# Optimization experiments

Measured on AMD Instinct MI355X. Metric: run time of the kernel, lower is better.

## Reference

```python
import jax, jax.numpy as jnp
import numpy as np

B, F, U, O, A, H = 8192, 1024, 512, 3, 6, 4  # batch, features, nb_units, nb_opponents, actions, heads
HD = U // H  # head dim


def setup_inputs() -> dict:
    key = jax.random.key(0)
    ks = jax.random.split(key, 12)
    s = 0.02
    rn = lambda k, shape: jax.random.normal(k, shape, jnp.float32) * s
    return {
        "features": jax.random.normal(ks[0], (B, F), jnp.float32),
        # agent latent Linear
        "W_al": rn(ks[1], (U, F)), "b_al": jnp.zeros((U,), jnp.float32),
        # MultiheadAttention in_proj (q,k,v stacked) and out_proj
        "W_in": rn(ks[2], (3 * U, U)), "b_in": jnp.zeros((3 * U,), jnp.float32),
        "W_out": rn(ks[3], (U, U)), "b_out": jnp.zeros((U,), jnp.float32),
        # agent head / policy / value
        "W_ah": rn(ks[4], (U, 2 * U)), "b_ah": jnp.zeros((U,), jnp.float32),
        "W_ap": rn(ks[5], (A, U)), "b_ap": jnp.zeros((A,), jnp.float32),
        "W_av": rn(ks[6], (1, U)), "b_av": jnp.zeros((1,), jnp.float32),
        # per-opponent stacks: latent, head, policy, value
        "W_ol": rn(ks[7], (O, U, F)), "b_ol": jnp.zeros((O, U), jnp.float32),
        "W_oh": rn(ks[8], (O, U, U)), "b_oh": jnp.zeros((O, U), jnp.float32),
        "W_op": rn(ks[9], (O, A, U)), "b_op": jnp.zeros((O, A), jnp.float32),
        "W_ov": rn(ks[10], (O, 1, U)), "b_ov": jnp.zeros((O, 1), jnp.float32),
    }


def reference(features, W_al, b_al, W_in, b_in, W_out, b_out, W_ah, b_ah,
              W_ap, b_ap, W_av, b_av, W_ol, b_ol, W_oh, b_oh, W_op, b_op, W_ov, b_ov):
    elu = jax.nn.elu
    # agent + per-opponent latents (per-opponent linears as one grouped GEMM)
    agent_latent = elu(features @ W_al.T + b_al)                                # [B,U]
    opp_lat = elu(jnp.einsum('bf,ouf->obu', features, W_ol) + b_ol[:, None, :])  # [O,B,U]

    # torch.nn.MultiheadAttention: query=[1,B,U] (agent), key=value=[O,B,U] (opponents)
    Wq, Wk, Wv = W_in[:U], W_in[U:2 * U], W_in[2 * U:]
    bq, bk, bv = b_in[:U], b_in[U:2 * U], b_in[2 * U:]
    q = (agent_latent @ Wq.T + bq).reshape(B, H, HD) * (1.0 / np.sqrt(HD))      # [B,H,HD]
    k = (jnp.einsum('obu,vu->obv', opp_lat, Wk) + bk).reshape(O, B, H, HD)
    v = (jnp.einsum('obu,vu->obv', opp_lat, Wv) + bv).reshape(O, B, H, HD)
    scores = jnp.einsum('bhd,obhd->bho', q, k)                                  # [B,H,O]
    w = jax.nn.softmax(scores, axis=-1)
    attn = jnp.einsum('bho,obhd->bhd', w, v).reshape(B, U)
    attn_out = attn @ W_out.T + b_out                                           # [B,U]
    opponents_influences = w.mean(axis=1)                                       # [B,O] (avg over heads)

    # agent head / policy / value
    cat = jnp.concatenate([agent_latent, attn_out], axis=1)                     # [B,2U]
    agent_head = elu(cat @ W_ah.T + b_ah)
    agent_policy = agent_head @ W_ap.T + b_ap                                   # [B,A]
    agent_value = agent_head @ W_av.T + b_av                                    # [B,1]

    # per-opponent head / policy / value (grouped GEMMs)
    opp_heads = elu(jnp.einsum('obu,ovu->obv', opp_lat, W_oh) + b_oh[:, None, :])  # [O,B,U]
    opponents_policies = jnp.einsum('obu,oau->boa', opp_heads, W_op) + b_op[None]   # [B,O,A]
    opponents_values = jnp.einsum('obu,ocu->boc', opp_heads, W_ov) + b_ov[None]     # [B,O,1]

    return (agent_policy, agent_value, opponents_policies, opponents_values, opponents_influences)
```

## Files before the change

### kernel.cpp

```cpp
#include <hip/hip_runtime.h>

typedef unsigned short u16;
typedef __bf16 bf16x8 __attribute__((ext_vector_type(8)));
typedef float f32x4 __attribute__((ext_vector_type(4)));

#define Bsz 8192
#define Fdim 1024
#define Udim 512
#define Odim 3
#define Adim 6
#define Hdim 4

#define OFF_FEAT   0
#define OFF_WAL    8388608
#define OFF_WIN    8912896
#define OFF_WOUT   9699328
#define OFF_WAH    9961472
#define OFF_WOL    10485760
#define OFF_WOH    12058624
#define OFF_CAT    12845056
#define OFF_OPP    21233664
#define OFF_Q      33816576
#define OFF_KV     38010880
#define OFF_ATT    63176704
#define OFF_AGH    67371008
#define OFF_OPH    71565312

#define OUT_AP 0
#define OUT_AV 49152
#define OUT_OP 57344
#define OUT_OV 204800
#define OUT_IN 229376

__device__ __forceinline__ u16 f2bf(float f) {
  return __builtin_bit_cast(u16, (__bf16)f);
}
__device__ __forceinline__ float bf2f(u16 u) {
  return (float)__builtin_bit_cast(__bf16, u);
}

__device__ __forceinline__ void gload16(const u16* g, u16* s) {
  __builtin_amdgcn_global_load_lds(
      (const __attribute__((address_space(1))) unsigned int*)g,
      (__attribute__((address_space(3))) unsigned int*)s, 16, 0, 0);
}

#define CV_E0 2097152
#define CV_E1 2228224
#define CV_E2 2424832
#define CV_E3 2490368
#define CV_E4 2621440
#define CV_E5 3014656
#define CV_E6 3211264
__global__ __launch_bounds__(256) void convert_all(
    const float* __restrict__ f, const float* __restrict__ wal,
    const float* __restrict__ win, const float* __restrict__ wout,
    const float* __restrict__ wah, const float* __restrict__ wol,
    const float* __restrict__ woh, u16* __restrict__ dst) {
  int i = blockIdx.x * 256 + threadIdx.x;
  if (i >= CV_E6) return;
  const float* src;
  int base;
  if (i < CV_E0)      { src = f;    base = 0; }
  else if (i < CV_E1) { src = wal;  base = CV_E0; }
  else if (i < CV_E2) { src = win;  base = CV_E1; }
  else if (i < CV_E3) { src = wout; base = CV_E2; }
  else if (i < CV_E4) { src = wah;  base = CV_E3; }
  else if (i < CV_E5) { src = wol;  base = CV_E4; }
  else                { src = woh;  base = CV_E5; }
  float4 v = ((const float4*)src)[i - base];
  ushort4 o;
  o.x = f2bf(v.x); o.y = f2bf(v.y); o.z = f2bf(v.z); o.w = f2bf(v.w);
  ((ushort4*)dst)[i] = o;
}

template <int BN, bool ELU>
__global__ __launch_bounds__(256) void gemm_bt(
    const u16* __restrict__ A, const u16* __restrict__ Bw, u16* __restrict__ C,
    const float* __restrict__ bias, int K, int lda, int ldb, int ldc,
    long sAz, long sBz, long sCz, int sbz, float scale) {
  constexpr int BM = 128, BK = 32;
  constexpr int NI = BN / 32;
  __shared__ __align__(16) u16 As[BM * BK];
  __shared__ __align__(16) u16 Bs[BN * BK];
  const int wave = threadIdx.x >> 6, lane = threadIdx.x & 63;
  const int z = blockIdx.z;
  A += (size_t)z * sAz;
  Bw += (size_t)z * sBz;
  C += (size_t)z * sCz;
  bias += (size_t)z * sbz;
  const int tM = blockIdx.y * BM, tN = blockIdx.x * BN;
  const int wr = wave >> 1, wc = wave & 1;

  f32x4 acc[4][NI];
#pragma unroll
  for (int i = 0; i < 4; i++)
#pragma unroll
    for (int j = 0; j < NI; j++) acc[i][j] = (f32x4){0.f, 0.f, 0.f, 0.f};

  const int srow = lane >> 2;
  const int scol = (lane & 3) * 8;

  for (int k0 = 0; k0 < K; k0 += BK) {
    __syncthreads();
#pragma unroll
    for (int i = 0; i < 2; ++i) {
      int r = wave * 32 + i * 16;
      gload16(A + (size_t)(tM + r + srow) * lda + k0 + scol, &As[r * BK]);
    }
#pragma unroll
    for (int i = 0; i < BN / 64; ++i) {
      int r = (wave * (BN / 64) + i) * 16;
      gload16(Bw + (size_t)(tN + r + srow) * ldb + k0 + scol, &Bs[r * BK]);
    }
    __syncthreads();
    bf16x8 af[4], bfr[NI];
#pragma unroll
    for (int mi = 0; mi < 4; mi++)
      af[mi] = *(const bf16x8*)&As[(wr * 64 + mi * 16 + (lane & 15)) * BK + (lane >> 4) * 8];
#pragma unroll
    for (int ni = 0; ni < NI; ni++)
      bfr[ni] = *(const bf16x8*)&Bs[(wc * (BN / 2) + ni * 16 + (lane & 15)) * BK + (lane >> 4) * 8];
#pragma unroll
    for (int mi = 0; mi < 4; mi++)
#pragma unroll
      for (int ni = 0; ni < NI; ni++)
        acc[mi][ni] = __builtin_amdgcn_mfma_f32_16x16x32_bf16(af[mi], bfr[ni], acc[mi][ni], 0, 0, 0);
  }

#pragma unroll
  for (int ni = 0; ni < NI; ni++) {
    int col = tN + wc * (BN / 2) + ni * 16 + (lane & 15);
    float bv = bias[col];
#pragma unroll
    for (int mi = 0; mi < 4; mi++) {
      int row0 = tM + wr * 64 + mi * 16 + (lane >> 4) * 4;
#pragma unroll
      for (int r = 0; r < 4; r++) {
        float v = (acc[mi][ni][r] + bv) * scale;
        if (ELU) v = v > 0.f ? v : (__expf(v) - 1.f);
        C[(size_t)(row0 + r) * ldc + col] = f2bf(v);
      }
    }
  }
}

__global__ __launch_bounds__(256) void attn_kernel(
    const u16* __restrict__ q, const u16* __restrict__ kv,
    u16* __restrict__ attn, float* __restrict__ influ) {
  const int wave = threadIdx.x >> 6, lane = threadIdx.x & 63;
  const int b = blockIdx.x * 4 + wave;
  const size_t qb = (size_t)b * 512;
  float wacc0 = 0.f, wacc1 = 0.f, wacc2 = 0.f;
#pragma unroll
  for (int h = 0; h < 4; ++h) {
    const int off = h * 128 + lane * 2;
    ushort2 qu = *(const ushort2*)(q + qb + off);
    float qx = bf2f(qu.x), qy = bf2f(qu.y);
    float s[3];
#pragma unroll
    for (int o = 0; o < 3; ++o) {
      ushort2 ku = *(const ushort2*)(kv + (size_t)o * (Bsz * 1024) + (size_t)b * 1024 + off);
      float p = qx * bf2f(ku.x) + qy * bf2f(ku.y);
#pragma unroll
      for (int d = 32; d; d >>= 1) p += __shfl_xor(p, d, 64);
      s[o] = p;
    }
    float m = fmaxf(s[0], fmaxf(s[1], s[2]));
    float e0 = __expf(s[0] - m), e1 = __expf(s[1] - m), e2 = __expf(s[2] - m);
    float inv = 1.f / (e0 + e1 + e2);
    float w0 = e0 * inv, w1 = e1 * inv, w2 = e2 * inv;
    wacc0 += w0; wacc1 += w1; wacc2 += w2;
    float ax = 0.f, ay = 0.f;
#pragma unroll
    for (int o = 0; o < 3; ++o) {
      float w = (o == 0) ? w0 : (o == 1) ? w1 : w2;
      ushort2 vu = *(const ushort2*)(kv + (size_t)o * (Bsz * 1024) + (size_t)b * 1024 + 512 + off);
      ax += w * bf2f(vu.x);
      ay += w * bf2f(vu.y);
    }
    ushort2 st; st.x = f2bf(ax); st.y = f2bf(ay);
    *(ushort2*)(attn + qb + off) = st;
  }
  if (lane == 0) {
    influ[b * 3 + 0] = wacc0 * 0.25f;
    influ[b * 3 + 1] = wacc1 * 0.25f;
    influ[b * 3 + 2] = wacc2 * 0.25f;
  }
}

__global__ __launch_bounds__(256) void heads_kernel(
    const u16* __restrict__ ah, const u16* __restrict__ oh,
    const float* __restrict__ Wap, const float* __restrict__ bap,
    const float* __restrict__ Wav, const float* __restrict__ bav,
    const float* __restrict__ Wop, const float* __restrict__ bop,
    const float* __restrict__ Wov, const float* __restrict__ bov,
    float* __restrict__ out) {
  __shared__ float sW[14336];
  for (int i = threadIdx.x; i < 14336; i += 256) {
    int s = i / 3584, rem = i - s * 3584;
    float v;
    if (s == 0) {
      v = (rem < 3072) ? Wap[rem] : Wav[rem - 3072];
    } else {
      int o = s - 1;
      v = (rem < 3072) ? Wop[o * 3072 + rem] : Wov[o * 512 + (rem - 3072)];
    }
    sW[i] = v;
  }
  __syncthreads();
  const int wave = threadIdx.x >> 6, lane = threadIdx.x & 63;
  const int kq = lane & 7, r = lane >> 3;
  const int b = blockIdx.x * 32 + wave * 8 + r;

  const u16* srcs[4] = {ah + (size_t)b * 512,
                        oh + (size_t)b * 512,
                        oh + (size_t)(Bsz + b) * 512,
                        oh + (size_t)(2 * Bsz + b) * 512};
  bf16x8 a[4][8];
#pragma unroll
  for (int s = 0; s < 4; s++)
#pragma unroll
    for (int c = 0; c < 8; c++)
      a[s][c] = *(const bf16x8*)(srcs[s] + c * 64 + kq * 8);

#pragma unroll
  for (int s = 0; s < 4; s++) {
#pragma unroll
    for (int p = 0; p < 7; p++) {
      const float* w = &sW[s * 3584 + p * 512 + kq * 8];
      float acc = 0.f;
#pragma unroll
      for (int c = 0; c < 8; c++) {
#pragma unroll
        for (int j = 0; j < 8; j++)
          acc += (float)a[s][c][j] * w[c * 64 + j];
      }
      acc += __shfl_xor(acc, 1, 64);
      acc += __shfl_xor(acc, 2, 64);
      acc += __shfl_xor(acc, 4, 64);
      if (kq == p) {
        if (s == 0) {
          if (p < 6) out[OUT_AP + b * 6 + p] = acc + bap[p];
          else       out[OUT_AV + b] = acc + bav[0];
        } else {
          int o = s - 1;
          if (p < 6) out[OUT_OP + b * 18 + o * 6 + p] = acc + bop[o * 6 + p];
          else       out[OUT_OV + b * 3 + o] = acc + bov[o];
        }
      }
    }
  }
}

extern "C" void kernel_launch(void* const* d_in, const int* in_sizes, int n_in,
                              void* d_out, int out_size, void* d_ws, size_t ws_size,
                              hipStream_t stream) {
  (void)in_sizes; (void)n_in; (void)out_size; (void)ws_size;
  const float* f     = (const float*)d_in[0];
  const float* W_al  = (const float*)d_in[1];
  const float* b_al  = (const float*)d_in[2];
  const float* W_in  = (const float*)d_in[3];
  const float* b_in  = (const float*)d_in[4];
  const float* W_out = (const float*)d_in[5];
  const float* b_out = (const float*)d_in[6];
  const float* W_ah  = (const float*)d_in[7];
  const float* b_ah  = (const float*)d_in[8];
  const float* W_ap  = (const float*)d_in[9];
  const float* b_ap  = (const float*)d_in[10];
  const float* W_av  = (const float*)d_in[11];
  const float* b_av  = (const float*)d_in[12];
  const float* W_ol  = (const float*)d_in[13];
  const float* b_ol  = (const float*)d_in[14];
  const float* W_oh  = (const float*)d_in[15];
  const float* b_oh  = (const float*)d_in[16];
  const float* W_op  = (const float*)d_in[17];
  const float* b_op  = (const float*)d_in[18];
  const float* W_ov  = (const float*)d_in[19];
  const float* b_ov  = (const float*)d_in[20];
  float* out = (float*)d_out;
  u16* ws = (u16*)d_ws;

  u16* feat = ws + OFF_FEAT;
  u16* wal  = ws + OFF_WAL;
  u16* win  = ws + OFF_WIN;
  u16* wout = ws + OFF_WOUT;
  u16* wah  = ws + OFF_WAH;
  u16* wol  = ws + OFF_WOL;
  u16* woh  = ws + OFF_WOH;
  u16* cat  = ws + OFF_CAT;
  u16* opp  = ws + OFF_OPP;
  u16* qb   = ws + OFF_Q;
  u16* kvb  = ws + OFF_KV;
  u16* att  = ws + OFF_ATT;
  u16* agh  = ws + OFF_AGH;
  u16* oph  = ws + OFF_OPH;

  convert_all<<<12544, 256, 0, stream>>>(f, W_al, W_in, W_out, W_ah, W_ol, W_oh, ws);

  gemm_bt<64, true><<<dim3(8, 64, 1), 256, 0, stream>>>(
      feat, wal, cat, b_al, 1024, 1024, 1024, 1024, 0, 0, 0, 0, 1.f);
  gemm_bt<128, true><<<dim3(12, 64, 1), 256, 0, stream>>>(
      feat, wol, opp, b_ol, 1024, 1024, 1024, 1536, 0, 0, 0, 0, 1.f);
  gemm_bt<64, false><<<dim3(8, 64, 1), 256, 0, stream>>>(
      cat, win, qb, b_in, 512, 1024, 512, 512, 0, 0, 0, 0, 0.08838834764831845f);
  gemm_bt<128, false><<<dim3(8, 64, 3), 256, 0, stream>>>(
      opp, win + 262144, kvb, b_in + 512, 512, 1536, 512, 1024, 512, 0, 8388608, 0, 1.f);

  attn_kernel<<<2048, 256, 0, stream>>>(qb, kvb, att, out + OUT_IN);

  gemm_bt<64, false><<<dim3(8, 64, 1), 256, 0, stream>>>(
      att, wout, cat + 512, b_out, 512, 512, 512, 1024, 0, 0, 0, 0, 1.f);
  gemm_bt<64, true><<<dim3(8, 64, 1), 256, 0, stream>>>(
      cat, wah, agh, b_ah, 1024, 1024, 1024, 512, 0, 0, 0, 0, 1.f);
  gemm_bt<128, true><<<dim3(4, 64, 3), 256, 0, stream>>>(
      opp, woh, oph, b_oh, 512, 1536, 512, 512, 512, 262144, 4194304, 512, 1.f);

  heads_kernel<<<256, 256, 0, stream>>>(agh, oph, W_ap, b_ap, W_av, b_av,
                                        W_op, b_op, W_ov, b_ov, out);
}
```

Measured before the change: 354.7 us.

## Fuse agent and opponent latent GEMMs and rework GEMM kernel with XCD swizzle

Concatenates W_al and W_ol into one weight so agent and opponent latents come from a single GEMM over features. The GEMM kernel now uses fixed 128x128 tiles, an XCD-aware block index remap, and a dual-A-source K split so the agent-head GEMM reads latent and attention output directly without a concat copy. It also uses an LDS layout matching the MFMA fragment and vectorized epilogue stores with split biases. This removes one pass over features and the concat write, at the cost of a more complex kernel and fewer blocks for some GEMMs.

New measurement: 406.7 us. 14.7% more time.

```diff
diff --git a/kernel.cpp b/kernel.cpp
--- a/kernel.cpp
+++ b/kernel.cpp
@@ -5,24 +5,18 @@
 typedef float f32x4 __attribute__((ext_vector_type(4)));
 
 #define Bsz 8192
-#define Fdim 1024
-#define Udim 512
-#define Odim 3
-#define Adim 6
-#define Hdim 4
 
 #define OFF_FEAT   0
-#define OFF_WAL    8388608
-#define OFF_WIN    8912896
-#define OFF_WOUT   9699328
-#define OFF_WAH    9961472
-#define OFF_WOL    10485760
+#define OFF_WCOMB  8388608
+#define OFF_WIN    10485760
+#define OFF_WOUT   11272192
+#define OFF_WAH    11534336
 #define OFF_WOH    12058624
-#define OFF_CAT    12845056
-#define OFF_OPP    21233664
-#define OFF_Q      33816576
-#define OFF_KV     38010880
-#define OFF_ATT    63176704
+#define OFF_LAT    12845056
+#define OFF_Q      29622272
+#define OFF_KV     33816576
+#define OFF_ATT    58982400
+#define OFF_AO     63176704
 #define OFF_AGH    67371008
 #define OFF_OPH    71565312
 
@@ -47,15 +41,15 @@
 
 #define CV_E0 2097152
 #define CV_E1 2228224
-#define CV_E2 2424832
-#define CV_E3 2490368
-#define CV_E4 2621440
+#define CV_E2 2621440
+#define CV_E3 2818048
+#define CV_E4 2883584
 #define CV_E5 3014656
 #define CV_E6 3211264
 __global__ __launch_bounds__(256) void convert_all(
     const float* __restrict__ f, const float* __restrict__ wal,
-    const float* __restrict__ win, const float* __restrict__ wout,
-    const float* __restrict__ wah, const float* __restrict__ wol,
+    const float* __restrict__ wol, const float* __restrict__ win,
+    const float* __restrict__ wout, const float* __restrict__ wah,
     const float* __restrict__ woh, u16* __restrict__ dst) {
   int i = blockIdx.x * 256 + threadIdx.x;
   if (i >= CV_E6) return;
@@ -63,10 +57,10 @@
   int base;
   if (i < CV_E0)      { src = f;    base = 0; }
   else if (i < CV_E1) { src = wal;  base = CV_E0; }
-  else if (i < CV_E2) { src = win;  base = CV_E1; }
-  else if (i < CV_E3) { src = wout; base = CV_E2; }
-  else if (i < CV_E4) { src = wah;  base = CV_E3; }
-  else if (i < CV_E5) { src = wol;  base = CV_E4; }
+  else if (i < CV_E2) { src = wol;  base = CV_E1; }
+  else if (i < CV_E3) { src = win;  base = CV_E2; }
+  else if (i < CV_E4) { src = wout; base = CV_E3; }
+  else if (i < CV_E5) { src = wah;  base = CV_E4; }
   else                { src = woh;  base = CV_E5; }
   float4 v = ((const float4*)src)[i - base];
   ushort4 o;
@@ -74,73 +68,103 @@
   ((ushort4*)dst)[i] = o;
 }
 
-template <int BN, bool ELU>
-__global__ __launch_bounds__(256) void gemm_bt(
-    const u16* __restrict__ A, const u16* __restrict__ Bw, u16* __restrict__ C,
-    const float* __restrict__ bias, int K, int lda, int ldb, int ldc,
-    long sAz, long sBz, long sCz, int sbz, float scale) {
-  constexpr int BM = 128, BK = 32;
-  constexpr int NI = BN / 32;
-  __shared__ __align__(16) u16 As[BM * BK];
-  __shared__ __align__(16) u16 Bs[BN * BK];
+template <bool ELU>
+__global__ __launch_bounds__(256) void gemm_v2(
+    const u16* __restrict__ A, const u16* __restrict__ A2,
+    const u16* __restrict__ Bw, u16* __restrict__ C,
+    const float* __restrict__ bias, const float* __restrict__ bias2,
+    int K, int ksplit, int bsplit, int lda, int lda2, int ldb, int ldc,
+    long sAz, long sBz, long sCz, int sbz, float scale, int nxsh) {
+  __shared__ __align__(16) u16 S[8192];
   const int wave = threadIdx.x >> 6, lane = threadIdx.x & 63;
-  const int z = blockIdx.z;
-  A += (size_t)z * sAz;
+  const int l15 = lane & 15, l4 = lane >> 4;
+
+  const int flat = blockIdx.x;
+  const int xcd = flat & 7, s = flat >> 3;
+  const int x = s & ((1 << nxsh) - 1);
+  const int yz = ((s >> nxsh) << 3) | xcd;
+  const int y = yz & 63, z = yz >> 6;
+  const int tM = y * 128, tN = x * 128;
+
+  A  += (size_t)z * sAz;
+  A2 += (size_t)z * sAz;
   Bw += (size_t)z * sBz;
-  C += (size_t)z * sCz;
-  bias += (size_t)z * sbz;
-  const int tM = blockIdx.y * BM, tN = blockIdx.x * BN;
+  C  += (size_t)z * sCz;
+  bias  += (size_t)z * sbz;
+  bias2 += (size_t)z * sbz;
+
+  const bool isA = wave < 2;
+  const int half = isA ? wave : wave - 2;
+  const int kch = l4 * 8;
+  const u16* p1[4];
+  const u16* p2[4];
+  u16* dst[4];
+#pragma unroll
+  for (int t = 0; t < 4; ++t) {
+    int rowt = (isA ? tM : tN) + half * 64 + t * 16 + l15;
+    if (isA) {
+      p1[t] = A + (size_t)rowt * lda + kch;
+      p2[t] = A2 + ((long)rowt * lda2 + kch - ksplit);
+      dst[t] = &S[(half * 4 + t) * 512];
+    } else {
+      p1[t] = Bw + (size_t)rowt * ldb + kch;
+      p2[t] = p1[t];
+      dst[t] = &S[4096 + (half * 4 + t) * 512];
+    }
+  }
+  const int kspl_eff = isA ? ksplit : (1 << 30);
+
   const int wr = wave >> 1, wc = wave & 1;
-
-  f32x4 acc[4][NI];
+  f32x4 acc[4][4];
 #pragma unroll
   for (int i = 0; i < 4; i++)
 #pragma unroll
-    for (int j = 0; j < NI; j++) acc[i][j] = (f32x4){0.f, 0.f, 0.f, 0.f};
-
-  const int srow = lane >> 2;
-  const int scol = (lane & 3) * 8;
-
-  for (int k0 = 0; k0 < K; k0 += BK) {
+    for (int j = 0; j < 4; j++) acc[i][j] = (f32x4){0.f, 0.f, 0.f, 0.f};
+
+  for (int k0 = 0; k0 < K; k0 += 32) {
     __syncthreads();
-#pragma unroll
-    for (int i = 0; i < 2; ++i) {
-      int r = wave * 32 + i * 16;
-      gload16(A + (size_t)(tM + r + srow) * lda + k0 + scol, &As[r * BK]);
-    }
-#pragma unroll
-    for (int i = 0; i < BN / 64; ++i) {
-      int r = (wave * (BN / 64) + i) * 16;
-      gload16(Bw + (size_t)(tN + r + srow) * ldb + k0 + scol, &Bs[r * BK]);
-    }
+    const bool first = k0 < kspl_eff;
+#pragma unroll
+    for (int t = 0; t < 4; ++t)
+      gload16((first ? p1[t] : p2[t]) + k0, dst[t]);
     __syncthreads();
-    bf16x8 af[4], bfr[NI];
+    bf16x8 af[4], bfr[4];
 #pragma unroll
     for (int mi = 0; mi < 4; mi++)
-      af[mi] = *(const bf16x8*)&As[(wr * 64 + mi * 16 + (lane & 15)) * BK + (lane >> 4) * 8];
-#pragma unroll
-    for (int ni = 0; ni < NI; ni++)
-      bfr[ni] = *(const bf16x8*)&Bs[(wc * (BN / 2) + ni * 16 + (lane & 15)) * BK + (lane >> 4) * 8];
+      af[mi] = *(const bf16x8*)&S[(wr * 4 + mi) * 512 + lane * 8];
+#pragma unroll
+    for (int ni = 0; ni < 4; ni++)
+      bfr[ni] = *(const bf16x8*)&S[4096 + (wc * 4 + ni) * 512 + lane * 8];
 #pragma unroll
     for (int mi = 0; mi < 4; mi++)
 #pragma unroll
-      for (int ni = 0; ni < NI; ni++)
-        acc[mi][ni] = __builtin_amdgcn_mfma_f32_16x16x32_bf16(af[mi], bfr[ni], acc[mi][ni], 0, 0, 0);
-  }
-
-#pragma unroll
-  for (int ni = 0; ni < NI; ni++) {
-    int col = tN + wc * (BN / 2) + ni * 16 + (lane & 15);
-    float bv = bias[col];
-#pragma unroll
-    for (int mi = 0; mi < 4; mi++) {
-      int row0 = tM + wr * 64 + mi * 16 + (lane >> 4) * 4;
-#pragma unroll
-      for (int r = 0; r < 4; r++) {
-        float v = (acc[mi][ni][r] + bv) * scale;
-        if (ELU) v = v > 0.f ? v : (__expf(v) - 1.f);
-        C[(size_t)(row0 + r) * ldc + col] = f2bf(v);
+      for (int ni = 0; ni < 4; ni++)
+        acc[mi][ni] = __builtin_amdgcn_mfma_f32_16x16x32_bf16(bfr[ni], af[mi], acc[mi][ni], 0, 0, 0);
+  }
+
+#pragma unroll
+  for (int mi = 0; mi < 4; mi++) {
+    const int row = tM + wr * 64 + mi * 16 + l15;
+    u16* crow = C + (size_t)row * ldc;
+#pragma unroll
+    for (int ni = 0; ni < 4; ni++) {
+      const int col0 = tN + wc * 64 + ni * 16 + l4 * 4;
+      const float* bp = (col0 < bsplit) ? bias + col0 : bias2 + (col0 - bsplit);
+      float4 bv = *(const float4*)bp;
+      f32x4 a = acc[mi][ni];
+      float v0 = (a[0] + bv.x) * scale;
+      float v1 = (a[1] + bv.y) * scale;
+      float v2 = (a[2] + bv.z) * scale;
+      float v3 = (a[3] + bv.w) * scale;
+      if (ELU) {
+        v0 = v0 > 0.f ? v0 : (__expf(v0) - 1.f);
+        v1 = v1 > 0.f ? v1 : (__expf(v1) - 1.f);
+        v2 = v2 > 0.f ? v2 : (__expf(v2) - 1.f);
+        v3 = v3 > 0.f ? v3 : (__expf(v3) - 1.f);
       }
+      ushort4 st;
+      st.x = f2bf(v0); st.y = f2bf(v1); st.z = f2bf(v2); st.w = f2bf(v3);
+      *(ushort4*)(crow + col0) = st;
     }
   }
 }
@@ -281,40 +305,45 @@
   float* out = (float*)d_out;
   u16* ws = (u16*)d_ws;
 
-  u16* feat = ws + OFF_FEAT;
-  u16* wal  = ws + OFF_WAL;
-  u16* win  = ws + OFF_WIN;
-  u16* wout = ws + OFF_WOUT;
-  u16* wah  = ws + OFF_WAH;
-  u16* wol  = ws + OFF_WOL;
-  u16* woh  = ws + OFF_WOH;
-  u16* cat  = ws + OFF_CAT;
-  u16* opp  = ws + OFF_OPP;
-  u16* qb   = ws + OFF_Q;
-  u16* kvb  = ws + OFF_KV;
-  u16* att  = ws + OFF_ATT;
-  u16* agh  = ws + OFF_AGH;
-  u16* oph  = ws + OFF_OPH;
-
-  convert_all<<<12544, 256, 0, stream>>>(f, W_al, W_in, W_out, W_ah, W_ol, W_oh, ws);
-
-  gemm_bt<64, true><<<dim3(8, 64, 1), 256, 0, stream>>>(
-      feat, wal, cat, b_al, 1024, 1024, 1024, 1024, 0, 0, 0, 0, 1.f);
-  gemm_bt<128, true><<<dim3(12, 64, 1), 256, 0, stream>>>(
-      feat, wol, opp, b_ol, 1024, 1024, 1024, 1536, 0, 0, 0, 0, 1.f);
-  gemm_bt<64, false><<<dim3(8, 64, 1), 256, 0, stream>>>(
-      cat, win, qb, b_in, 512, 1024, 512, 512, 0, 0, 0, 0, 0.08838834764831845f);
-  gemm_bt<128, false><<<dim3(8, 64, 3), 256, 0, stream>>>(
-      opp, win + 262144, kvb, b_in + 512, 512, 1536, 512, 1024, 512, 0, 8388608, 0, 1.f);
+  u16* feat  = ws + OFF_FEAT;
+  u16* wcomb = ws + OFF_WCOMB;
+  u16* win   = ws + OFF_WIN;
+  u16* wout  = ws + OFF_WOUT;
+  u16* wah   = ws + OFF_WAH;
+  u16* woh   = ws + OFF_WOH;
+  u16* lat   = ws + OFF_LAT;
+  u16* qb    = ws + OFF_Q;
+  u16* kvb   = ws + OFF_KV;
+  u16* att   = ws + OFF_ATT;
+  u16* ao    = ws + OFF_AO;
+  u16* agh   = ws + OFF_AGH;
+  u16* oph   = ws + OFF_OPH;
+
+  const int BIG = 1 << 30;
+
+  convert_all<<<12544, 256, 0, stream>>>(f, W_al, W_ol, W_in, W_out, W_ah, W_oh, ws);
+
+  gemm_v2<true><<<1024, 256, 0, stream>>>(
+      feat, feat, wcomb, lat, b_al, b_ol, 1024, BIG, 512,
+      1024, 1024, 1024, 2048, 0, 0, 0, 0, 1.f, 4);
+  gemm_v2<false><<<256, 256, 0, stream>>>(
+      lat, lat, win, qb, b_in, b_in, 512, BIG, BIG,
+      2048, 2048, 512, 512, 0, 0, 0, 0, 0.08838834764831845f, 2);
+  gemm_v2<false><<<1536, 256, 0, stream>>>(
+      lat + 512, lat + 512, win + 262144, kvb, b_in + 512, b_in + 512,
+      512, BIG, BIG, 2048, 2048, 512, 1024, 512, 0, 8388608, 0, 1.f, 3);
 
   attn_kernel<<<2048, 256, 0, stream>>>(qb, kvb, att, out + OUT_IN);
 
-  gemm_bt<64, false><<<dim3(8, 64, 1), 256, 0, stream>>>(
-      att, wout, cat + 512, b_out, 512, 512, 512, 1024, 0, 0, 0, 0, 1.f);
-  gemm_bt<64, true><<<dim3(8, 64, 1), 256, 0, stream>>>(
-      cat, wah, agh, b_ah, 1024, 1024, 1024, 512, 0, 0, 0, 0, 1.f);
-  gemm_bt<128, true><<<dim3(4, 64, 3), 256, 0, stream>>>(
-      opp, woh, oph, b_oh, 512, 1536, 512, 512, 512, 262144, 4194304, 512, 1.f);
+  gemm_v2<false><<<256, 256, 0, stream>>>(
+      att, att, wout, ao, b_out, b_out, 512, BIG, BIG,
+      512, 512, 512, 512, 0, 0, 0, 0, 1.f, 2);
+  gemm_v2<true><<<256, 256, 0, stream>>>(
+      lat, ao, wah, agh, b_ah, b_ah, 1024, 512, BIG,
+      2048, 512, 1024, 512, 0, 0, 0, 0, 1.f, 2);
+  gemm_v2<true><<<768, 256, 0, stream>>>(
+      lat + 512, lat + 512, woh, oph, b_oh, b_oh, 512, BIG, BIG,
+      2048, 2048, 512, 512, 512, 262144, 4194304, 512, 1.f, 2);
 
   heads_kernel<<<256, 256, 0, stream>>>(agh, oph, W_ap, b_ap, W_av, b_av,
                                         W_op, b_op, W_ov, b_ov, out);
```
